# Kernel optimization log

Measured on AMD Instinct MI355X. Metric: run time of the kernel, lower is better.

The kernel has to match this reference:

```python
import jax, jax.numpy as jnp
import numpy as np

N_NODES = 100000
N_EDGES = 3200000
N_FEAT = 500
HIDDEN = 128
N_CLASSES = 64
K_LAYERS = 10
ALPHA = 0.1


def setup_inputs() -> dict:
    key = jax.random.key(0)
    k_x, k_e, k_w1, k_b1, k_w2, k_b2 = jax.random.split(key, 6)
    x = jax.random.normal(k_x, (N_NODES, N_FEAT), dtype=jnp.float32)
    edge_index = jax.random.randint(k_e, (2, N_EDGES), 0, N_NODES, dtype=jnp.int64)
    # Linear layers (torch nn.Linear default init ~ U(-1/sqrt(fan_in), 1/sqrt(fan_in)))
    s1 = 1.0 / np.sqrt(N_FEAT)
    s2 = 1.0 / np.sqrt(HIDDEN)
    W1 = jax.random.uniform(k_w1, (N_FEAT, HIDDEN), jnp.float32, -s1, s1)
    b1 = jax.random.uniform(k_b1, (HIDDEN,), jnp.float32, -s1, s1)
    W2 = jax.random.uniform(k_w2, (HIDDEN, N_CLASSES), jnp.float32, -s2, s2)
    b2 = jax.random.uniform(k_b2, (N_CLASSES,), jnp.float32, -s2, s2)
    return {"x": x, "edge_index": edge_index, "W1": W1, "b1": b1, "W2": W2, "b2": b2}


def reference(x, edge_index, W1, b1, W2, b2):
    n = x.shape[0]
    # MLP: Linear -> ReLU -> Linear
    h = jnp.maximum(x @ W1 + b1, 0.0) @ W2 + b2  # [N, C]

    # GCN symmetric normalization with self-loops (PyG APPNP / gcn_norm)
    loops = jnp.arange(n, dtype=edge_index.dtype)
    src = jnp.concatenate([edge_index[0], loops])
    dst = jnp.concatenate([edge_index[1], loops])
    deg = jax.ops.segment_sum(jnp.ones_like(dst, dtype=h.dtype), dst, num_segments=n)
    dinv = jnp.where(deg > 0, jax.lax.rsqrt(deg), 0.0)
    norm = dinv[src] * dinv[dst]  # [E+N]

    h0 = h

    def step(z, _):
        msgs = z[src] * norm[:, None]                       # gather over edges
        agg = jax.ops.segment_sum(msgs, dst, num_segments=n)  # scatter-add
        z_new = (1.0 - ALPHA) * agg + ALPHA * h0
        return z_new, None

    z, _ = jax.lax.scan(step, h0, None, length=K_LAYERS)
    return jax.nn.softmax(z, axis=1)
```

## Files before the change

kernel.cpp:

```cpp
#include <hip/hip_runtime.h>
#include <hip/hip_bf16.h>
#include <hip/hip_fp16.h>

#define N_NODES   100000
#define N_EDGES   3200000
#define N_FEAT    500
#define HIDDEN    128
#define N_CLASSES 64
#define K_LAYERS  10
#define NBUCK     98

typedef __attribute__((ext_vector_type(8))) short bf16x8;
typedef __attribute__((ext_vector_type(4))) float f32x4;

__device__ inline ushort f2bf_rn(float f) {
  unsigned u = __float_as_uint(f);
  unsigned r = (u + 0x7FFFu + ((u >> 16) & 1u)) >> 16;
  return (ushort)r;
}
__device__ inline float bf2f(ushort h) {
  return __uint_as_float(((unsigned)h) << 16);
}
__device__ inline float2 h2f2(unsigned u) {
  __half2 h = *(__half2*)&u;
  return make_float2(__low2float(h), __high2float(h));
}
__device__ inline unsigned f2h2(float a, float b) {
  __half2 h = __floats2half2_rn(a, b);
  return *(unsigned*)&h;
}


__global__ __launch_bounds__(256) void bucket_count_k(const int* __restrict__ dst,
                                                      int* __restrict__ bucket_cnt) {
  __shared__ int h[128];
  int t = threadIdx.x;
  if (t < 128) h[t] = 0;
  __syncthreads();
  for (int e = blockIdx.x * 256 + t; e < N_EDGES; e += gridDim.x * 256)
    atomicAdd(&h[dst[e] >> 10], 1);
  __syncthreads();
  if (t < 128 && h[t]) atomicAdd(&bucket_cnt[t], h[t]);
}

__global__ __launch_bounds__(128) void bucket_scan_k(const int* __restrict__ bucket_cnt,
                                                     int* __restrict__ bucket_base,
                                                     int* __restrict__ bcur,
                                                     int* __restrict__ offs) {
  __shared__ int sm[128];
  int t = threadIdx.x;
  int c = bucket_cnt[t];
  sm[t] = c;
  __syncthreads();
  for (int d = 1; d < 128; d <<= 1) {
    int v = (t >= d) ? sm[t - d] : 0;
    __syncthreads();
    sm[t] += v;
    __syncthreads();
  }
  int ex = sm[t] - c;
  bucket_base[t] = ex;
  bcur[t] = ex;
  if (t == 127) bucket_base[128] = ex + c;
  if (t == 0) offs[N_NODES] = N_EDGES;
}

#define BIN_CHUNK 12800
__global__ __launch_bounds__(256) void bin_scatter_k(const int* __restrict__ src,
                                                     const int* __restrict__ dst,
                                                     int* __restrict__ bcur,
                                                     int* __restrict__ binned) {
  __shared__ int h[128];
  __shared__ int hbase[128];
  int t = threadIdx.x;
  int e0 = blockIdx.x * BIN_CHUNK;
  int e1 = min(e0 + BIN_CHUNK, N_EDGES);
  if (t < 128) h[t] = 0;
  __syncthreads();
  for (int e = e0 + t; e < e1; e += 256) atomicAdd(&h[dst[e] >> 10], 1);
  __syncthreads();
  if (t < 128) {
    int c = h[t];
    hbase[t] = c ? atomicAdd(&bcur[t], c) : 0;
  }
  __syncthreads();
  if (t < 128) h[t] = 0;
  __syncthreads();
  for (int e = e0 + t; e < e1; e += 256) {
    int d = dst[e];
    int b = d >> 10;
    int pos = hbase[b] + atomicAdd(&h[b], 1);
    binned[pos] = (src[e] & 0x1FFFF) | ((d & 1023) << 17);
  }
}

__global__ __launch_bounds__(256) void bucket_fill_k(const int* __restrict__ binned,
                                                     const int* __restrict__ bucket_base,
                                                     int* __restrict__ offs,
                                                     float* __restrict__ dinv,
                                                     int* __restrict__ csr4) {
  __shared__ int cnt[1024];
  __shared__ int tsum[256];
  int b = blockIdx.x;
  int base = bucket_base[b];
  int nE = bucket_base[b + 1] - base;
  int node0 = b << 10;
  int nN = min(1024, N_NODES - node0);
  int t = threadIdx.x;
  #pragma unroll
  for (int i = 0; i < 4; ++i) cnt[t + i * 256] = 0;
  __syncthreads();
  for (int i = t; i < nE; i += 256) atomicAdd(&cnt[binned[base + i] >> 17], 1);
  __syncthreads();
  int c0 = cnt[4 * t], c1 = cnt[4 * t + 1], c2 = cnt[4 * t + 2], c3 = cnt[4 * t + 3];
  int s = c0 + c1 + c2 + c3;
  tsum[t] = s;
  __syncthreads();
  for (int d = 1; d < 256; d <<= 1) {
    int v = (t >= d) ? tsum[t - d] : 0;
    __syncthreads();
    tsum[t] += v;
    __syncthreads();
  }
  int run = tsum[t] - s;
  int p0 = run, p1 = run + c0, p2 = p1 + c1, p3 = p2 + c2;
  if (4 * t + 0 < nN) { offs[node0 + 4 * t + 0] = base + p0; dinv[node0 + 4 * t + 0] = rsqrtf(c0 + 1.f); }
  if (4 * t + 1 < nN) { offs[node0 + 4 * t + 1] = base + p1; dinv[node0 + 4 * t + 1] = rsqrtf(c1 + 1.f); }
  if (4 * t + 2 < nN) { offs[node0 + 4 * t + 2] = base + p2; dinv[node0 + 4 * t + 2] = rsqrtf(c2 + 1.f); }
  if (4 * t + 3 < nN) { offs[node0 + 4 * t + 3] = base + p3; dinv[node0 + 4 * t + 3] = rsqrtf(c3 + 1.f); }
  __syncthreads();
  cnt[4 * t] = p0; cnt[4 * t + 1] = p1; cnt[4 * t + 2] = p2; cnt[4 * t + 3] = p3;
  __syncthreads();
  for (int i = t; i < nE; i += 256) {
    int rec = binned[base + i];
    int p = base + atomicAdd(&cnt[rec >> 17], 1);
    csr4[p] = rec & 0x1FFFF;
  }
}

__global__ void prep_wt_k(const float* __restrict__ W, ushort* __restrict__ hi,
                          ushort* __restrict__ lo, int K, int N, int KPAD) {
  int idx = blockIdx.x * 256 + threadIdx.x;
  if (idx >= N * KPAD) return;
  int n = idx / KPAD, k = idx - n * KPAD;
  float v = (k < K) ? W[(size_t)k * N + n] : 0.f;
  ushort h = f2bf_rn(v);
  ushort l = f2bf_rn(v - bf2f(h));
  hi[idx] = h;
  lo[idx] = l;
}

template<int BN, int KTOT, int KPAD, bool RELU>
__global__ __launch_bounds__(256, 2) void mfma_gemm_k(
    const float* __restrict__ A, const ushort* __restrict__ BThi,
    const ushort* __restrict__ BTlo, const float* __restrict__ bias,
    float* __restrict__ C, int M) {
  constexpr int BK = 64;
  constexpr int NF = BN / 32;
  __shared__ __align__(16) ushort sm[(2 * 128 + 2 * BN) * BK];
  ushort* Ahi = sm;
  ushort* Alo = sm + 128 * BK;
  ushort* Bhi = sm + 2 * 128 * BK;
  ushort* Blo = Bhi + BN * BK;

  int tid = threadIdx.x;
  int lane = tid & 63, wid = tid >> 6;
  int wm = wid >> 1, wn = wid & 1;
  int lrow = lane & 15, lg = lane >> 4;
  int row0 = blockIdx.x * 128;

  f32x4 acc[4][NF];
  #pragma unroll
  for (int m = 0; m < 4; ++m)
    #pragma unroll
    for (int n = 0; n < NF; ++n) acc[m][n] = (f32x4){0.f, 0.f, 0.f, 0.f};

  for (int kc = 0; kc < KPAD; kc += BK) {
    __syncthreads();
    #pragma unroll
    for (int i = 0; i < 8; ++i) {
      int c = tid + i * 256;
      int r = c >> 4, k4 = (c & 15) << 2;
      int gr = row0 + r, gk = kc + k4;
      float4 v = make_float4(0.f, 0.f, 0.f, 0.f);
      if (gr < M) {
        if (gk + 3 < KTOT) {
          v = *(const float4*)(A + (size_t)gr * KTOT + gk);
        } else {
          float* vp = &v.x;
          #pragma unroll
          for (int e = 0; e < 4; ++e)
            if (gk + e < KTOT) vp[e] = A[(size_t)gr * KTOT + gk + e];
        }
      }
      ushort h0 = f2bf_rn(v.x), h1 = f2bf_rn(v.y), h2 = f2bf_rn(v.z), h3 = f2bf_rn(v.w);
      ushort l0 = f2bf_rn(v.x - bf2f(h0)), l1 = f2bf_rn(v.y - bf2f(h1));
      ushort l2 = f2bf_rn(v.z - bf2f(h2)), l3 = f2bf_rn(v.w - bf2f(h3));
      int chunk = k4 >> 3, sub = k4 & 4;
      int ad = r * 64 + ((chunk << 3) ^ ((r & 7) << 3)) + sub;
      *(ushort4*)(Ahi + ad) = make_ushort4(h0, h1, h2, h3);
      *(ushort4*)(Alo + ad) = make_ushort4(l0, l1, l2, l3);
    }
    #pragma unroll
    for (int i = 0; i < BN * 8 / 256; ++i) {
      int c = tid + i * 256;
      int n = c >> 3, ch = c & 7;
      int gk = kc + ch * 8;
      int ad = n * 64 + ((ch << 3) ^ ((n & 7) << 3));
      *(uint4*)(Bhi + ad) = *(const uint4*)(BThi + (size_t)n * KPAD + gk);
      *(uint4*)(Blo + ad) = *(const uint4*)(BTlo + (size_t)n * KPAD + gk);
    }
    __syncthreads();
    #pragma unroll
    for (int ks = 0; ks < 2; ++ks) {
      bf16x8 ah[4], al[4], bh[NF], bl[NF];
      #pragma unroll
      for (int m = 0; m < 4; ++m) {
        int r = wm * 64 + m * 16 + lrow;
        int ad = r * 64 + (((ks * 4 + lg) << 3) ^ ((r & 7) << 3));
        ah[m] = *(const bf16x8*)(Ahi + ad);
        al[m] = *(const bf16x8*)(Alo + ad);
      }
      #pragma unroll
      for (int n = 0; n < NF; ++n) {
        int r = wn * (BN / 2) + n * 16 + lrow;
        int ad = r * 64 + (((ks * 4 + lg) << 3) ^ ((r & 7) << 3));
        bh[n] = *(const bf16x8*)(Bhi + ad);
        bl[n] = *(const bf16x8*)(Blo + ad);
      }
      #pragma unroll
      for (int m = 0; m < 4; ++m)
        #pragma unroll
        for (int n = 0; n < NF; ++n) {
          acc[m][n] = __builtin_amdgcn_mfma_f32_16x16x32_bf16(ah[m], bh[n], acc[m][n], 0, 0, 0);
          acc[m][n] = __builtin_amdgcn_mfma_f32_16x16x32_bf16(ah[m], bl[n], acc[m][n], 0, 0, 0);
          acc[m][n] = __builtin_amdgcn_mfma_f32_16x16x32_bf16(al[m], bh[n], acc[m][n], 0, 0, 0);
        }
    }
  }
  #pragma unroll
  for (int m = 0; m < 4; ++m)
    #pragma unroll
    for (int n = 0; n < NF; ++n) {
      int gcol = wn * (BN / 2) + n * 16 + lrow;
      float bb = bias[gcol];
      #pragma unroll
      for (int r = 0; r < 4; ++r) {
        int grow = row0 + wm * 64 + m * 16 + lg * 4 + r;
        if (grow < M) {
          float v = acc[m][n][r] + bb;
          if (RELU) v = fmaxf(v, 0.f);
          C[(size_t)grow * BN + gcol] = v;
        }
      }
    }
}

__global__ __launch_bounds__(256) void conv_y0_k(const float* __restrict__ h0,
                                                 const float* __restrict__ dinv,
                                                 uint2* __restrict__ y16) {
  int i = blockIdx.x * 256 + threadIdx.x;
  if (i >= N_NODES * 16) return;
  int node = i >> 4;
  float dv = dinv[node];
  float4 h4 = ((const float4*)h0)[i];
  y16[i] = make_uint2(f2h2(dv * h4.x, dv * h4.y), f2h2(dv * h4.z, dv * h4.w));
}

template<bool OUT32>
__global__ __launch_bounds__(256) void prop_k(const uint2* __restrict__ yin,
                                              void* __restrict__ out,
                                              const float* __restrict__ h0,
                                              const float* __restrict__ dinv,
                                              const int* __restrict__ offs,
                                              const int* __restrict__ csr4) {
  int lane = threadIdx.x & 63;
  int wid = threadIdx.x >> 6;
  int node = (blockIdx.x << 2) + wid;
  if (node >= N_NODES) return;
  int grp = lane >> 4;
  int lc = lane & 15;

  float4 acc = make_float4(0.f, 0.f, 0.f, 0.f);
  int beg = offs[node], end = offs[node + 1];
  for (int e = beg; e < end; e += 64) {
    int s = (e + lane < end) ? csr4[e + lane] : N_NODES;
    int cnt = min(64, end - e);
    for (int j = 0; j < cnt; j += 32) {
      int sr[8];
      uint2 g[8];
      #pragma unroll
      for (int q = 0; q < 8; ++q) sr[q] = __shfl(s, j + 4 * q + grp);
      #pragma unroll
      for (int q = 0; q < 8; ++q) g[q] = yin[(size_t)sr[q] * 16 + lc];
      #pragma unroll
      for (int q = 0; q < 8; ++q) {
        float2 a = h2f2(g[q].x), b = h2f2(g[q].y);
        acc.x += a.x; acc.y += a.y; acc.z += b.x; acc.w += b.y;
      }
    }
  }
  #pragma unroll
  for (int off = 16; off <= 32; off <<= 1) {
    acc.x += __shfl_xor(acc.x, off);
    acc.y += __shfl_xor(acc.y, off);
    acc.z += __shfl_xor(acc.z, off);
    acc.w += __shfl_xor(acc.w, off);
  }
  if (grp == 0) {
    uint2 gs = yin[(size_t)node * 16 + lc];
    float2 a = h2f2(gs.x), b = h2f2(gs.y);
    acc.x += a.x; acc.y += a.y; acc.z += b.x; acc.w += b.y;
    float dv = dinv[node];
    float4 h4 = ((const float4*)h0)[(size_t)node * 16 + lc];
    float4 z;
    z.x = 0.9f * dv * acc.x + 0.1f * h4.x;
    z.y = 0.9f * dv * acc.y + 0.1f * h4.y;
    z.z = 0.9f * dv * acc.z + 0.1f * h4.z;
    z.w = 0.9f * dv * acc.w + 0.1f * h4.w;
    if (OUT32) {
      ((float4*)out)[(size_t)node * 16 + lc] = z;
    } else {
      ((uint2*)out)[(size_t)node * 16 + lc] =
          make_uint2(f2h2(dv * z.x, dv * z.y), f2h2(dv * z.z, dv * z.w));
    }
  }
}

__global__ __launch_bounds__(256) void softmax_k(const float* __restrict__ z,
                                                 float* __restrict__ out) {
  int lane = threadIdx.x & 63;
  int row = (blockIdx.x * 256 + threadIdx.x) >> 6;
  if (row >= N_NODES) return;
  float v = z[(size_t)row * 64 + lane];
  float m = v;
  #pragma unroll
  for (int o = 32; o > 0; o >>= 1) m = fmaxf(m, __shfl_xor(m, o));
  float ev = __expf(v - m);
  float s = ev;
  #pragma unroll
  for (int o = 32; o > 0; o >>= 1) s += __shfl_xor(s, o);
  out[(size_t)row * 64 + lane] = ev / s;
}

extern "C" void kernel_launch(void* const* d_in, const int* in_sizes, int n_in,
                              void* d_out, int out_size, void* d_ws, size_t ws_size,
                              hipStream_t stream) {
  const float* x  = (const float*)d_in[0];
  const int*   ei = (const int*)d_in[1];
  const float* W1 = (const float*)d_in[2];
  const float* b1 = (const float*)d_in[3];
  const float* W2 = (const float*)d_in[4];
  const float* b2 = (const float*)d_in[5];
  const int* src = ei;
  const int* dst = ei + N_EDGES;

  char* w = (char*)d_ws;
  int*    csr4  = (int*)w;
  float*  H     = (float*)(w + 12800000);
  uint2*  zA16  = (uint2*)(w + 12800000);
  uint2*  zB16  = (uint2*)(w + 25700000);
  float*  zF32  = (float*)(w + 38600000);
  int*    binned = (int*)(w + 38600000);
  float*  dinv  = (float*)(w + 64500000);
  int*    offs  = (int*)(w + 65000000);
  int*    bucket_cnt  = (int*)(w + 66000000);
  int*    bucket_base = (int*)(w + 66002048);
  int*    bcur        = (int*)(w + 66004096);
  ushort* w1thi = (ushort*)(w + 66500000);
  ushort* w1tlo = (ushort*)(w + 66700000);
  ushort* w2thi = (ushort*)(w + 66900000);
  ushort* w2tlo = (ushort*)(w + 67000000);
  float* h0 = (float*)d_out;

  hipMemsetAsync(bucket_cnt, 0, 128 * 4, stream);

  bucket_count_k<<<512, 256, 0, stream>>>(dst, bucket_cnt);
  bucket_scan_k<<<1, 128, 0, stream>>>(bucket_cnt, bucket_base, bcur, offs);
  bin_scatter_k<<<N_EDGES / BIN_CHUNK, 256, 0, stream>>>(src, dst, bcur, binned);
  bucket_fill_k<<<NBUCK, 256, 0, stream>>>(binned, bucket_base, offs, dinv, csr4);

  prep_wt_k<<<(128 * 512 + 255) / 256, 256, 0, stream>>>(W1, w1thi, w1tlo, 500, 128, 512);
  prep_wt_k<<<(64 * 128 + 255) / 256, 256, 0, stream>>>(W2, w2thi, w2tlo, 128, 64, 128);
  mfma_gemm_k<128, 500, 512, true><<<(N_NODES + 127) / 128, 256, 0, stream>>>(
      x, w1thi, w1tlo, b1, H, N_NODES);
  mfma_gemm_k<64, 128, 128, false><<<(N_NODES + 127) / 128, 256, 0, stream>>>(
      H, w2thi, w2tlo, b2, h0, N_NODES);

  hipMemsetAsync((char*)zA16 + (size_t)N_NODES * 128, 0, 128, stream);
  hipMemsetAsync((char*)zB16 + (size_t)N_NODES * 128, 0, 128, stream);

  conv_y0_k<<<(N_NODES * 16 + 255) / 256, 256, 0, stream>>>(h0, dinv, zA16);

  const uint2* zi = zA16;
  uint2* zo = zB16;
  for (int it = 0; it < K_LAYERS - 1; ++it) {
    prop_k<false><<<(N_NODES + 3) / 4, 256, 0, stream>>>(zi, (void*)zo, h0, dinv, offs, csr4);
    zi = zo;
    zo = (zo == zA16) ? zB16 : zA16;
  }
  prop_k<true><<<(N_NODES + 3) / 4, 256, 0, stream>>>(zi, (void*)zF32, h0, dinv, offs, csr4);

  softmax_k<<<(N_NODES * 64) / 256, 256, 0, stream>>>(zF32, (float*)d_out);
}
```

Measured before the change: 1.062 ms.

## Prefetch next GEMM K-tile into registers while computing current tile

Splits the GEMM tile staging into a global-to-register load and a register-to-LDS write. The next K-chunk's global loads are issued before the MFMA work on the current chunk, hiding global memory latency behind compute. In exchange it holds extra registers for the prefetched A (8 float4) and B fragments, which may hurt occupancy under launch_bounds(256,2).

```diff
diff --git a/kernel.cpp b/kernel.cpp
--- a/kernel.cpp
+++ b/kernel.cpp
@@ -157,6 +157,8 @@
     float* __restrict__ C, int M) {
   constexpr int BK = 64;
   constexpr int NF = BN / 32;
+  constexpr int NB = BN * 8 / 256;
+  constexpr int NS = KPAD / BK;
   __shared__ __align__(16) ushort sm[(2 * 128 + 2 * BN) * BK];
   ushort* Ahi = sm;
   ushort* Alo = sm + 128 * BK;
@@ -175,8 +177,10 @@
     #pragma unroll
     for (int n = 0; n < NF; ++n) acc[m][n] = (f32x4){0.f, 0.f, 0.f, 0.f};
 
-  for (int kc = 0; kc < KPAD; kc += BK) {
-    __syncthreads();
+  float4 aR[8];
+  uint4 bhR[NB], blR[NB];
+
+  auto load_st = [&](int kc) {
     #pragma unroll
     for (int i = 0; i < 8; ++i) {
       int c = tid + i * 256;
@@ -193,6 +197,24 @@
             if (gk + e < KTOT) vp[e] = A[(size_t)gr * KTOT + gk + e];
         }
       }
+      aR[i] = v;
+    }
+    #pragma unroll
+    for (int i = 0; i < NB; ++i) {
+      int c = tid + i * 256;
+      int n = c >> 3, ch = c & 7;
+      int gk = kc + ch * 8;
+      bhR[i] = *(const uint4*)(BThi + (size_t)n * KPAD + gk);
+      blR[i] = *(const uint4*)(BTlo + (size_t)n * KPAD + gk);
+    }
+  };
+
+  auto write_st = [&]() {
+    #pragma unroll
+    for (int i = 0; i < 8; ++i) {
+      int c = tid + i * 256;
+      int r = c >> 4, k4 = (c & 15) << 2;
+      float4 v = aR[i];
       ushort h0 = f2bf_rn(v.x), h1 = f2bf_rn(v.y), h2 = f2bf_rn(v.z), h3 = f2bf_rn(v.w);
       ushort l0 = f2bf_rn(v.x - bf2f(h0)), l1 = f2bf_rn(v.y - bf2f(h1));
       ushort l2 = f2bf_rn(v.z - bf2f(h2)), l3 = f2bf_rn(v.w - bf2f(h3));
@@ -202,15 +224,22 @@
       *(ushort4*)(Alo + ad) = make_ushort4(l0, l1, l2, l3);
     }
     #pragma unroll
-    for (int i = 0; i < BN * 8 / 256; ++i) {
+    for (int i = 0; i < NB; ++i) {
       int c = tid + i * 256;
       int n = c >> 3, ch = c & 7;
-      int gk = kc + ch * 8;
       int ad = n * 64 + ((ch << 3) ^ ((n & 7) << 3));
-      *(uint4*)(Bhi + ad) = *(const uint4*)(BThi + (size_t)n * KPAD + gk);
-      *(uint4*)(Blo + ad) = *(const uint4*)(BTlo + (size_t)n * KPAD + gk);
-    }
-    __syncthreads();
+      *(uint4*)(Bhi + ad) = bhR[i];
+      *(uint4*)(Blo + ad) = blR[i];
+    }
+  };
+
+  load_st(0);
+  write_st();
+  __syncthreads();
+
+  #pragma unroll 1
+  for (int s = 0; s < NS; ++s) {
+    if (s + 1 < NS) load_st((s + 1) * BK);
     #pragma unroll
     for (int ks = 0; ks < 2; ++ks) {
       bf16x8 ah[4], al[4], bh[NF], bl[NF];
@@ -237,7 +266,13 @@
           acc[m][n] = __builtin_amdgcn_mfma_f32_16x16x32_bf16(al[m], bh[n], acc[m][n], 0, 0, 0);
         }
     }
-  }
+    if (s + 1 < NS) {
+      __syncthreads();
+      write_st();
+      __syncthreads();
+    }
+  }
+
   #pragma unroll
   for (int m = 0; m < 4; ++m)
     #pragma unroll
```

Result: slower. 1.122 ms (+5.6%).

## Replace split-bf16 GEMMs with single fp16 MFMA and async LDS weight staging

Applied to the files above, without the earlier changes.

Both MLP GEMMs drop the three-MFMA hi/lo bf16 split and use a single fp16 MFMA, with A loaded straight from global into registers instead of through LDS. Weights are pre-swizzled into fp16 and double-buffered into LDS via global_load_lds. The hidden activation H is now stored as fp16, halving its write and read traffic. This cuts MFMA work and LDS traffic for the GEMM stage but loses precision relative to the emulated-fp32 path.

```diff
diff --git a/kernel.cpp b/kernel.cpp
--- a/kernel.cpp
+++ b/kernel.cpp
@@ -10,17 +10,9 @@
 #define K_LAYERS  10
 #define NBUCK     98
 
-typedef __attribute__((ext_vector_type(8))) short bf16x8;
 typedef __attribute__((ext_vector_type(4))) float f32x4;
-
-__device__ inline ushort f2bf_rn(float f) {
-  unsigned u = __float_as_uint(f);
-  unsigned r = (u + 0x7FFFu + ((u >> 16) & 1u)) >> 16;
-  return (ushort)r;
-}
-__device__ inline float bf2f(ushort h) {
-  return __uint_as_float(((unsigned)h) << 16);
-}
+typedef __attribute__((ext_vector_type(8))) _Float16 f16x8;
+
 __device__ inline float2 h2f2(unsigned u) {
   __half2 h = *(__half2*)&u;
   return make_float2(__low2float(h), __high2float(h));
@@ -138,122 +130,143 @@
   }
 }
 
-__global__ void prep_wt_k(const float* __restrict__ W, ushort* __restrict__ hi,
-                          ushort* __restrict__ lo, int K, int N, int KPAD) {
-  int idx = blockIdx.x * 256 + threadIdx.x;
-  if (idx >= N * KPAD) return;
-  int n = idx / KPAD, k = idx - n * KPAD;
-  float v = (k < K) ? W[(size_t)k * N + n] : 0.f;
-  ushort h = f2bf_rn(v);
-  ushort l = f2bf_rn(v - bf2f(h));
-  hi[idx] = h;
-  lo[idx] = l;
-}
-
-template<int BN, int KTOT, int KPAD, bool RELU>
-__global__ __launch_bounds__(256, 2) void mfma_gemm_k(
-    const float* __restrict__ A, const ushort* __restrict__ BThi,
-    const ushort* __restrict__ BTlo, const float* __restrict__ bias,
-    float* __restrict__ C, int M) {
+__global__ void prep_wsw_k(const float* __restrict__ W, ushort* __restrict__ Bsw,
+                           int KTOT, int BN, int KPAD) {
+  int g = blockIdx.x * 256 + threadIdx.x;
+  if (g >= BN * KPAD) return;
+  int chunk = BN * 64;
+  int s = g / chunk;
+  int r = g - s * chunk;
+  int c = r >> 6;
+  int q = r & 63;
+  int X = (q >> 3) ^ (c & 7);
+  int e = q & 7;
+  int k = s * 64 + X * 8 + e;
+  float v = (k < KTOT) ? W[(size_t)k * BN + c] : 0.f;
+  _Float16 hv = (_Float16)v;
+  Bsw[g] = *(ushort*)&hv;
+}
+
+template<int BN, int KTOT, int KPAD, bool RELU, bool A16, bool C16>
+__device__ __forceinline__ void gemm_core(const void* Ain, const ushort* Bsw,
+                                          const float* bias, void* Cout, int M) {
   constexpr int BK = 64;
-  constexpr int NF = BN / 32;
-  __shared__ __align__(16) ushort sm[(2 * 128 + 2 * BN) * BK];
-  ushort* Ahi = sm;
-  ushort* Alo = sm + 128 * BK;
-  ushort* Bhi = sm + 2 * 128 * BK;
-  ushort* Blo = Bhi + BN * BK;
+  constexpr int NS = KPAD / BK;
+  constexpr int NF = BN / 16;
+  constexpr int CHUNK = BN * BK;
+  constexpr int NL = CHUNK * 2 / (16 * 256);
+  __shared__ __align__(16) ushort Bl[2][CHUNK];
 
   int tid = threadIdx.x;
-  int lane = tid & 63, wid = tid >> 6;
-  int wm = wid >> 1, wn = wid & 1;
+  int lane = tid & 63, w = tid >> 6;
   int lrow = lane & 15, lg = lane >> 4;
-  int row0 = blockIdx.x * 128;
-
-  f32x4 acc[4][NF];
-  #pragma unroll
-  for (int m = 0; m < 4; ++m)
+  int row0 = blockIdx.x * 128 + w * 32;
+
+  const float* A32 = (const float*)Ain;
+  const ushort* Ah = (const ushort*)Ain;
+
+  f32x4 acc[2][NF];
+  #pragma unroll
+  for (int m = 0; m < 2; ++m)
     #pragma unroll
     for (int n = 0; n < NF; ++n) acc[m][n] = (f32x4){0.f, 0.f, 0.f, 0.f};
 
-  for (int kc = 0; kc < KPAD; kc += BK) {
-    __syncthreads();
+  #define STAGE(s, buf)                                                   \
+    {                                                                     \
+      const ushort* gp = Bsw + (size_t)(s) * CHUNK;                       \
+      _Pragma("unroll")                                                   \
+      for (int i = 0; i < NL; ++i) {                                      \
+        int o = (tid + i * 256) * 8;                                      \
+        __builtin_amdgcn_global_load_lds(gp + o, &Bl[buf][o], 16, 0, 0);  \
+      }                                                                   \
+    }
+
+  STAGE(0, 0);
+  asm volatile("s_waitcnt vmcnt(0)" ::: "memory");
+  __syncthreads();
+
+  #pragma unroll 1
+  for (int s = 0; s < NS; ++s) {
+    int cur = s & 1;
+    if (s + 1 < NS) STAGE(s + 1, cur ^ 1);
+    int kc = s * BK;
     #pragma unroll
-    for (int i = 0; i < 8; ++i) {
-      int c = tid + i * 256;
-      int r = c >> 4, k4 = (c & 15) << 2;
-      int gr = row0 + r, gk = kc + k4;
-      float4 v = make_float4(0.f, 0.f, 0.f, 0.f);
-      if (gr < M) {
-        if (gk + 3 < KTOT) {
-          v = *(const float4*)(A + (size_t)gr * KTOT + gk);
+    for (int ks = 0; ks < 2; ++ks) {
+      f16x8 af[2];
+      #pragma unroll
+      for (int m = 0; m < 2; ++m) {
+        int r = row0 + m * 16 + lrow;
+        int rc = r < M ? r : M - 1;
+        int k0 = kc + ks * 32 + lg * 8;
+        if (A16) {
+          af[m] = *(const f16x8*)(Ah + (size_t)rc * KPAD + k0);
         } else {
-          float* vp = &v.x;
-          #pragma unroll
-          for (int e = 0; e < 4; ++e)
-            if (gk + e < KTOT) vp[e] = A[(size_t)gr * KTOT + gk + e];
+          const float* ap = A32 + (size_t)rc * KTOT + k0;
+          f16x8 h;
+          if (k0 + 7 < KTOT) {
+            float4 f0 = *(const float4*)ap;
+            float4 f1 = *(const float4*)(ap + 4);
+            h[0] = (_Float16)f0.x; h[1] = (_Float16)f0.y;
+            h[2] = (_Float16)f0.z; h[3] = (_Float16)f0.w;
+            h[4] = (_Float16)f1.x; h[5] = (_Float16)f1.y;
+            h[6] = (_Float16)f1.z; h[7] = (_Float16)f1.w;
+          } else {
+            #pragma unroll
+            for (int e = 0; e < 8; ++e)
+              h[e] = (_Float16)((k0 + e < KTOT) ? ap[e] : 0.f);
+          }
+          af[m] = h;
         }
       }
-      ushort h0 = f2bf_rn(v.x), h1 = f2bf_rn(v.y), h2 = f2bf_rn(v.z), h3 = f2bf_rn(v.w);
-      ushort l0 = f2bf_rn(v.x - bf2f(h0)), l1 = f2bf_rn(v.y - bf2f(h1));
-      ushort l2 = f2bf_rn(v.z - bf2f(h2)), l3 = f2bf_rn(v.w - bf2f(h3));
-      int chunk = k4 >> 3, sub = k4 & 4;
-      int ad = r * 64 + ((chunk << 3) ^ ((r & 7) << 3)) + sub;
-      *(ushort4*)(Ahi + ad) = make_ushort4(h0, h1, h2, h3);
-      *(ushort4*)(Alo + ad) = make_ushort4(l0, l1, l2, l3);
+      #pragma unroll
+      for (int n = 0; n < NF; ++n) {
+        int c = n * 16 + lrow;
+        int ad = c * 64 + ((((ks << 2) + lg) ^ (c & 7)) << 3);
+        f16x8 bf = *(const f16x8*)(&Bl[cur][ad]);
+        #pragma unroll
+        for (int m = 0; m < 2; ++m)
+          acc[m][n] = __builtin_amdgcn_mfma_f32_16x16x32_f16(af[m], bf, acc[m][n], 0, 0, 0);
+      }
     }
-    #pragma unroll
-    for (int i = 0; i < BN * 8 / 256; ++i) {
-      int c = tid + i * 256;
-      int n = c >> 3, ch = c & 7;
-      int gk = kc + ch * 8;
-      int ad = n * 64 + ((ch << 3) ^ ((n & 7) << 3));
-      *(uint4*)(Bhi + ad) = *(const uint4*)(BThi + (size_t)n * KPAD + gk);
-      *(uint4*)(Blo + ad) = *(const uint4*)(BTlo + (size_t)n * KPAD + gk);
-    }
+    asm volatile("s_waitcnt vmcnt(0)" ::: "memory");
     __syncthreads();
-    #pragma unroll
-    for (int ks = 0; ks < 2; ++ks) {
-      bf16x8 ah[4], al[4], bh[NF], bl[NF];
-      #pragma unroll
-      for (int m = 0; m < 4; ++m) {
-        int r = wm * 64 + m * 16 + lrow;
-        int ad = r * 64 + (((ks * 4 + lg) << 3) ^ ((r & 7) << 3));
-        ah[m] = *(const bf16x8*)(Ahi + ad);
-        al[m] = *(const bf16x8*)(Alo + ad);
-      }
-      #pragma unroll
-      for (int n = 0; n < NF; ++n) {
-        int r = wn * (BN / 2) + n * 16 + lrow;
-        int ad = r * 64 + (((ks * 4 + lg) << 3) ^ ((r & 7) << 3));
-        bh[n] = *(const bf16x8*)(Bhi + ad);
-        bl[n] = *(const bf16x8*)(Blo + ad);
-      }
-      #pragma unroll
-      for (int m = 0; m < 4; ++m)
-        #pragma unroll
-        for (int n = 0; n < NF; ++n) {
-          acc[m][n] = __builtin_amdgcn_mfma_f32_16x16x32_bf16(ah[m], bh[n], acc[m][n], 0, 0, 0);
-          acc[m][n] = __builtin_amdgcn_mfma_f32_16x16x32_bf16(ah[m], bl[n], acc[m][n], 0, 0, 0);
-          acc[m][n] = __builtin_amdgcn_mfma_f32_16x16x32_bf16(al[m], bh[n], acc[m][n], 0, 0, 0);
-        }
-    }
-  }
-  #pragma unroll
-  for (int m = 0; m < 4; ++m)
+  }
+  #undef STAGE
+
+  #pragma unroll
+  for (int m = 0; m < 2; ++m)
     #pragma unroll
     for (int n = 0; n < NF; ++n) {
-      int gcol = wn * (BN / 2) + n * 16 + lrow;
-      float bb = bias[gcol];
-      #pragma unroll
-      for (int r = 0; r < 4; ++r) {
-        int grow = row0 + wm * 64 + m * 16 + lg * 4 + r;
+      int c = n * 16 + lrow;
+      float bb = bias[c];
+      #pragma unroll
+      for (int r4 = 0; r4 < 4; ++r4) {
+        int grow = row0 + m * 16 + lg * 4 + r4;
         if (grow < M) {
-          float v = acc[m][n][r] + bb;
+          float v = acc[m][n][r4] + bb;
           if (RELU) v = fmaxf(v, 0.f);
-          C[(size_t)grow * BN + gcol] = v;
+          if (C16) {
+            _Float16 hv = (_Float16)v;
+            ((ushort*)Cout)[(size_t)grow * BN + c] = *(ushort*)&hv;
+          } else {
+            ((float*)Cout)[(size_t)grow * BN + c] = v;
+          }
         }
       }
     }
+}
+
+__global__ __launch_bounds__(256, 2) void gemm1_k(const float* __restrict__ A,
+                                                  const ushort* __restrict__ Bsw,
+                                                  const float* __restrict__ bias,
+                                                  ushort* __restrict__ C, int M) {
+  gemm_core<128, 500, 512, true, false, true>(A, Bsw, bias, C, M);
+}
+__global__ __launch_bounds__(256, 2) void gemm2_k(const ushort* __restrict__ A,
+                                                  const ushort* __restrict__ Bsw,
+                                                  const float* __restrict__ bias,
+                                                  float* __restrict__ C, int M) {
+  gemm_core<64, 128, 128, false, true, false>(A, Bsw, bias, C, M);
 }
 
 __global__ __launch_bounds__(256) void conv_y0_k(const float* __restrict__ h0,
@@ -357,7 +370,7 @@
 
   char* w = (char*)d_ws;
   int*    csr4  = (int*)w;
-  float*  H     = (float*)(w + 12800000);
+  ushort* H     = (ushort*)(w + 12800000);
   uint2*  zA16  = (uint2*)(w + 12800000);
   uint2*  zB16  = (uint2*)(w + 25700000);
   float*  zF32  = (float*)(w + 38600000);
@@ -367,10 +380,8 @@
   int*    bucket_cnt  = (int*)(w + 66000000);
   int*    bucket_base = (int*)(w + 66002048);
   int*    bcur        = (int*)(w + 66004096);
-  ushort* w1thi = (ushort*)(w + 66500000);
-  ushort* w1tlo = (ushort*)(w + 66700000);
-  ushort* w2thi = (ushort*)(w + 66900000);
-  ushort* w2tlo = (ushort*)(w + 67000000);
+  ushort* w1sw  = (ushort*)(w + 66500000);
+  ushort* w2sw  = (ushort*)(w + 66700000);
   float* h0 = (float*)d_out;
 
   hipMemsetAsync(bucket_cnt, 0, 128 * 4, stream);
@@ -380,12 +391,10 @@
   bin_scatter_k<<<N_EDGES / BIN_CHUNK, 256, 0, stream>>>(src, dst, bcur, binned);
   bucket_fill_k<<<NBUCK, 256, 0, stream>>>(binned, bucket_base, offs, dinv, csr4);
 
-  prep_wt_k<<<(128 * 512 + 255) / 256, 256, 0, stream>>>(W1, w1thi, w1tlo, 500, 128, 512);
-  prep_wt_k<<<(64 * 128 + 255) / 256, 256, 0, stream>>>(W2, w2thi, w2tlo, 128, 64, 128);
-  mfma_gemm_k<128, 500, 512, true><<<(N_NODES + 127) / 128, 256, 0, stream>>>(
-      x, w1thi, w1tlo, b1, H, N_NODES);
-  mfma_gemm_k<64, 128, 128, false><<<(N_NODES + 127) / 128, 256, 0, stream>>>(
-      H, w2thi, w2tlo, b2, h0, N_NODES);
+  prep_wsw_k<<<(128 * 512 + 255) / 256, 256, 0, stream>>>(W1, w1sw, 500, 128, 512);
+  prep_wsw_k<<<(64 * 128 + 255) / 256, 256, 0, stream>>>(W2, w2sw, 128, 64, 128);
+  gemm1_k<<<(N_NODES + 127) / 128, 256, 0, stream>>>(x, w1sw, b1, H, N_NODES);
+  gemm2_k<<<(N_NODES + 127) / 128, 256, 0, stream>>>(H, w2sw, b2, h0, N_NODES);
 
   hipMemsetAsync((char*)zA16 + (size_t)N_NODES * 128, 0, 128, stream);
   hipMemsetAsync((char*)zB16 + (size_t)N_NODES * 128, 0, 128, stream);
```

After: 993.8 us. 1.07x faster.
